# Kernel tuning notes

Hardware: AMD Instinct MI355X
Metric: run time of the kernel (lower is better)

Reference implementation:

```python
import jax, jax.numpy as jnp
import numpy as np
from itertools import product

DEG = 3
N_COMPLEX = 8

def monomial_powers(deg: int, n_complex: int = 8) -> np.ndarray:
    out = [a for a in product(range(deg + 1), repeat=n_complex) if sum(a) <= deg]
    return np.asarray(out, dtype=np.int32)

POWERS = monomial_powers(DEG, N_COMPLEX)  # (K, 8)
K = POWERS.shape[0]                       # 165 for deg=3
MAXP = int(POWERS.max())                  # 3


def z_monomials(q):
    """q (B,16) real -> z^alpha (B,K) complex, z_k = q[:,k] + i q[:,k+8]."""
    x, y = q[:, :N_COMPLEX], q[:, N_COMPLEX:]
    z = jax.lax.complex(x, y)  # (B, 8)
    # power ladders z^0..z^MAXP : (B, 8, MAXP+1)
    cur = jnp.ones_like(z)
    ladders = [cur]
    for _ in range(MAXP):
        cur = cur * z
        ladders.append(cur)
    lad = jnp.stack(ladders, axis=-1)  # (B, 8, MAXP+1)
    mon = jnp.ones((q.shape[0], K), dtype=z.dtype)
    for c in range(N_COMPLEX):  # fixed 8 iterations (structural)
        mon = mon * lad[:, c, POWERS[:, c]]  # gather (B, K)
    return mon


def setup_inputs() -> dict:
    key = jax.random.key(0)
    kq, = jax.random.split(key, 1)
    B = 262144
    q = jax.random.normal(kq, (B, 16), dtype=jnp.float32)
    L_re = jnp.eye(K, dtype=jnp.float32)
    L_im = jnp.zeros((K, K), dtype=jnp.float32)
    return {"q": q, "L_re": L_re, "L_im": L_im}


def reference(q, L_re, L_im):
    # Cholesky-like factor L: strict lower triangles + softplus-positive diagonal
    Lr = jnp.tril(L_re, -1)
    Li = jnp.tril(L_im, -1)
    diag = jax.nn.softplus(jnp.diagonal(L_re)) + 0.001
    L = jax.lax.complex(Lr, Li) + jnp.diag(jax.lax.complex(diag, jnp.zeros_like(diag)))
    H = L @ L.conj().T                      # (K, K) Hermitian PSD
    z_a = z_monomials(q)                    # (B, K) complex64
    Hs = z_a @ H.T                          # (B, K)
    quad = jnp.sum(Hs * jnp.conj(z_a), axis=-1).real  # (B,)
    return jnp.log(quad + 1e-12)
```

## Files before the change

kernel.cpp:

```cpp
#include <hip/hip_runtime.h>
#include <hip/hip_bf16.h>
#include <utility>

#define DEV static __device__ __forceinline__

typedef __attribute__((ext_vector_type(8))) short bf16x8;
typedef __attribute__((ext_vector_type(4))) float f32x4;

constexpr int KM   = 165;
constexpr int IT   = 11;
constexpr int ITP  = 12;
constexpr int KS   = 6;
constexpr int NB   = ITP * KS * 64;
constexpr int ROWS = 64;

struct Pw { unsigned char p[8]; };
struct PwTab { Pw a[KM]; };
constexpr PwTab gen_powers() {
  PwTab t{};
  int idx = 0;
  for (int a0 = 0; a0 <= 3; ++a0)
  for (int a1 = 0; a1 <= 3-a0; ++a1)
  for (int a2 = 0; a2 <= 3-a0-a1; ++a2)
  for (int a3 = 0; a3 <= 3-a0-a1-a2; ++a3)
  for (int a4 = 0; a4 <= 3-a0-a1-a2-a3; ++a4)
  for (int a5 = 0; a5 <= 3-a0-a1-a2-a3-a4; ++a5)
  for (int a6 = 0; a6 <= 3-a0-a1-a2-a3-a4-a5; ++a6)
  for (int a7 = 0; a7 <= 3-a0-a1-a2-a3-a4-a5-a6; ++a7) {
    t.a[idx].p[0] = (unsigned char)a0; t.a[idx].p[1] = (unsigned char)a1;
    t.a[idx].p[2] = (unsigned char)a2; t.a[idx].p[3] = (unsigned char)a3;
    t.a[idx].p[4] = (unsigned char)a4; t.a[idx].p[5] = (unsigned char)a5;
    t.a[idx].p[6] = (unsigned char)a6; t.a[idx].p[7] = (unsigned char)a7;
    ++idx;
  }
  return t;
}
constexpr PwTab PW = gen_powers();

DEV unsigned int f2bf(float f) {
  unsigned int u = __builtin_bit_cast(unsigned int, f);
  u += 0x7fffu + ((u >> 16) & 1u);
  return u >> 16;
}
DEV unsigned int pack2_bits(float lo, float hi) { return f2bf(lo) | (f2bf(hi) << 16); }
DEV unsigned int pack2(float lo, float hi) {
  unsigned int r;
  asm("v_cvt_pk_bf16_f32 %0, %1, %2" : "=v"(r) : "v"(lo), "v"(hi));
  return r;
}
DEV float softplusf(float x) { return (x > 20.f) ? x : log1pf(expf(x)); }

template<int JJ, int C>
DEV void mono_step(float& r, float& i,
                   const float (&lx)[8][3], const float (&ly)[8][3]) {
  constexpr int pc = PW.a[JJ].p[C];
  if constexpr (pc > 0) {
    const float ar = lx[C][pc-1], ai = ly[C][pc-1];
    const float tr = r*ar - i*ai;
    i = r*ai + i*ar;
    r = tr;
  }
}
template<int JJ>
DEV void mono_eval(float& mr, float& mi,
                   const float (&lx)[8][3], const float (&ly)[8][3]) {
  float r = 1.f, i = 0.f;
  mono_step<JJ,0>(r,i,lx,ly); mono_step<JJ,1>(r,i,lx,ly);
  mono_step<JJ,2>(r,i,lx,ly); mono_step<JJ,3>(r,i,lx,ly);
  mono_step<JJ,4>(r,i,lx,ly); mono_step<JJ,5>(r,i,lx,ly);
  mono_step<JJ,6>(r,i,lx,ly); mono_step<JJ,7>(r,i,lx,ly);
  mr = r; mi = i;
}
template<int JJ>
DEV void mono_eval_guard(float& r, float& i,
                         const float (&lx)[8][3], const float (&ly)[8][3]) {
  if constexpr (JJ < KM) mono_eval<JJ>(r, i, lx, ly);
  else { r = 0.f; i = 0.f; }
}

template<int T, int... Us>
DEV void gen8(std::integer_sequence<int, Us...>, float (&mr)[8], float (&mi)[8],
              const float (&lx)[8][3], const float (&ly)[8][3]) {
  (mono_eval_guard<8*T + Us>(mr[Us], mi[Us], lx, ly), ...);
}
template<int T>
DEV void gen_chunk(const float (&lx)[8][3], const float (&ly)[8][3],
                   unsigned int* Xf, unsigned int* Yf, int mf, int r15) {
  constexpr int ksv = T >> 2;
  constexpr int gv  = T & 3;
  float mr[8], mi[8];
  gen8<T>(std::make_integer_sequence<int, 8>{}, mr, mi, lx, ly);
  uint4 ux, uy;
  ux.x = pack2(mr[0], mr[1]); ux.y = pack2(mr[2], mr[3]);
  ux.z = pack2(mr[4], mr[5]); ux.w = pack2(mr[6], mr[7]);
  uy.x = pack2(mi[0], mi[1]); uy.y = pack2(mi[2], mi[3]);
  uy.z = pack2(mi[4], mi[5]); uy.w = pack2(mi[6], mi[7]);
  const unsigned int off = (unsigned int)((mf*6 + ksv)*256 + gv*64 + r15*4);
  *(uint4*)&Xf[off] = ux;
  *(uint4*)&Yf[off] = uy;
}
template<int W, int... Ts>
DEV void gen_seq(std::integer_sequence<int, Ts...>,
                 const float (&lx)[8][3], const float (&ly)[8][3],
                 unsigned int* Xf, unsigned int* Yf, int mf, int r15) {
  (gen_chunk<6*W + Ts>(lx, ly, Xf, Yf, mf, r15), ...);
}
template<int W>
DEV void gen_wave(const float (&lx)[8][3], const float (&ly)[8][3],
                  unsigned int* Xf, unsigned int* Yf, int mf, int r15) {
  gen_seq<W>(std::make_integer_sequence<int, 6>{}, lx, ly, Xf, Yf, mf, r15);
}

__global__ void __launch_bounds__(256) poskahler_prep(
    const float* __restrict__ Lre, const float* __restrict__ Lim,
    uint4* __restrict__ bp, uint4* __restrict__ bq) {
  const int tid = blockIdx.x * 256 + threadIdx.x;
  if (tid >= NB) return;
  const int lane = tid & 63;
  const int it = (tid >> 6) / KS;
  const int ks = (tid >> 6) % KS;
  const int j  = it * 16 + (lane & 15);
  const int ib = ks * 32 + ((lane >> 4) << 3);
  float pr[8], qr[8];
#pragma unroll
  for (int e = 0; e < 8; ++e) { pr[e] = 0.f; qr[e] = 0.f; }
  if (j < KM) {
#pragma unroll
    for (int e = 0; e < 8; ++e) {
      const int i = ib + e;
      if (i < KM) {
        if (i > j)      { pr[e] = Lre[i*KM + j]; qr[e] = -Lim[i*KM + j]; }
        else if (i == j){ pr[e] = softplusf(Lre[j*KM + j]) + 0.001f; }
      }
    }
  }
  uint4 up, uq;
  up.x = pack2_bits(pr[0], pr[1]); up.y = pack2_bits(pr[2], pr[3]);
  up.z = pack2_bits(pr[4], pr[5]); up.w = pack2_bits(pr[6], pr[7]);
  uq.x = pack2_bits(qr[0], qr[1]); uq.y = pack2_bits(qr[2], qr[3]);
  uq.z = pack2_bits(qr[4], qr[5]); uq.w = pack2_bits(qr[6], qr[7]);
  bp[tid] = up;
  bq[tid] = uq;
}

template<int KSv>
DEV void load_tiles(const uint4* __restrict__ bp, const uint4* __restrict__ bq,
                    int wv, int lane, uint4 (&tp)[3], uint4 (&tq)[3]) {
#pragma unroll
  for (int ii = 0; ii < 3; ++ii) {
    const int it = 4*ii + wv;
    if (it <= 2*KSv + 1 && it < IT) {
      const int fs = (it*KS + KSv)*64 + lane;
      tp[ii] = bp[fs];
      tq[ii] = bq[fs];
    }
  }
}

template<int KSv>
DEV void compute_ks(const unsigned int* Xf, const unsigned int* Yf,
                    int wv, int lane,
                    const uint4 (&tp)[3], const uint4 (&tq)[3],
                    float (&aRe)[3][4][4], float (&aIm)[3][4][4]) {
  bf16x8 xf[4], yf[4];
#pragma unroll
  for (int mf = 0; mf < 4; ++mf) {
    const unsigned int off = (unsigned int)((mf*6 + KSv)*256) + (unsigned int)lane*4;
    xf[mf] = __builtin_bit_cast(bf16x8, *(const uint4*)&Xf[off]);
    yf[mf] = __builtin_bit_cast(bf16x8, *(const uint4*)&Yf[off]);
  }
#pragma unroll
  for (int ii = 0; ii < 3; ++ii) {
    const int it = 4*ii + wv;
    if (it <= 2*KSv + 1 && it < IT) {
      const uint4 up = tp[ii];
      const uint4 uq = tq[ii];
      uint4 un;
      un.x = uq.x ^ 0x80008000u; un.y = uq.y ^ 0x80008000u;
      un.z = uq.z ^ 0x80008000u; un.w = uq.w ^ 0x80008000u;
      const bf16x8 vp = __builtin_bit_cast(bf16x8, up);
      const bf16x8 vq = __builtin_bit_cast(bf16x8, uq);
      const bf16x8 vn = __builtin_bit_cast(bf16x8, un);
#pragma unroll
      for (int mf = 0; mf < 4; ++mf) {
        f32x4 cre = { aRe[ii][mf][0], aRe[ii][mf][1], aRe[ii][mf][2], aRe[ii][mf][3] };
        f32x4 cim = { aIm[ii][mf][0], aIm[ii][mf][1], aIm[ii][mf][2], aIm[ii][mf][3] };
        cre = __builtin_amdgcn_mfma_f32_16x16x32_bf16(xf[mf], vp, cre, 0, 0, 0);
        cre = __builtin_amdgcn_mfma_f32_16x16x32_bf16(yf[mf], vq, cre, 0, 0, 0);
        cim = __builtin_amdgcn_mfma_f32_16x16x32_bf16(yf[mf], vp, cim, 0, 0, 0);
        cim = __builtin_amdgcn_mfma_f32_16x16x32_bf16(xf[mf], vn, cim, 0, 0, 0);
#pragma unroll
        for (int rr = 0; rr < 4; ++rr) { aRe[ii][mf][rr] = cre[rr]; aIm[ii][mf][rr] = cim[rr]; }
      }
    }
  }
}

__global__ void __launch_bounds__(256, 2) poskahler_main(
    const float* __restrict__ q,
    const uint4* __restrict__ bp, const uint4* __restrict__ bq,
    float* __restrict__ out) {
  __shared__ __align__(16) unsigned int Xf[6144];
  __shared__ __align__(16) unsigned int Yf[6144];
  __shared__ float qpart[4][ROWS];

  const int t     = threadIdx.x;
  const int lane  = t & 63;
  const int wv    = t >> 6;
  const int bbase = blockIdx.x * ROWS;
  const int mf_r  = lane >> 4;
  const int r15   = lane & 15;

  const float* qr = q + (size_t)(bbase + lane) * 16;
  const float4 q0 = ((const float4*)qr)[0];
  const float4 q1 = ((const float4*)qr)[1];
  const float4 q2 = ((const float4*)qr)[2];
  const float4 q3 = ((const float4*)qr)[3];

  uint4 tpA[3] = {}, tqA[3] = {}, tpB[3] = {}, tqB[3] = {};
  load_tiles<0>(bp, bq, wv, lane, tpA, tqA);
  load_tiles<1>(bp, bq, wv, lane, tpB, tqB);

  {
    const float xs[8] = {q0.x,q0.y,q0.z,q0.w,q1.x,q1.y,q1.z,q1.w};
    const float ys[8] = {q2.x,q2.y,q2.z,q2.w,q3.x,q3.y,q3.z,q3.w};
    float lx[8][3], ly[8][3];
#pragma unroll
    for (int c = 0; c < 8; ++c) {
      const float xr = xs[c], yi = ys[c];
      lx[c][0] = xr;             ly[c][0] = yi;
      lx[c][1] = xr*xr - yi*yi;  ly[c][1] = 2.f*xr*yi;
      lx[c][2] = lx[c][1]*xr - ly[c][1]*yi;
      ly[c][2] = lx[c][1]*yi + ly[c][1]*xr;
    }
    switch (wv) {
      case 0: gen_wave<0>(lx, ly, Xf, Yf, mf_r, r15); break;
      case 1: gen_wave<1>(lx, ly, Xf, Yf, mf_r, r15); break;
      case 2: gen_wave<2>(lx, ly, Xf, Yf, mf_r, r15); break;
      default: gen_wave<3>(lx, ly, Xf, Yf, mf_r, r15); break;
    }
  }
  __syncthreads();

  float aRe[3][4][4], aIm[3][4][4];
#pragma unroll
  for (int ii = 0; ii < 3; ++ii)
#pragma unroll
    for (int mf = 0; mf < 4; ++mf)
#pragma unroll
      for (int rr = 0; rr < 4; ++rr) { aRe[ii][mf][rr] = 0.f; aIm[ii][mf][rr] = 0.f; }

  compute_ks<0>(Xf, Yf, wv, lane, tpA, tqA, aRe, aIm);
  load_tiles<2>(bp, bq, wv, lane, tpA, tqA);
  compute_ks<1>(Xf, Yf, wv, lane, tpB, tqB, aRe, aIm);
  load_tiles<3>(bp, bq, wv, lane, tpB, tqB);
  compute_ks<2>(Xf, Yf, wv, lane, tpA, tqA, aRe, aIm);
  load_tiles<4>(bp, bq, wv, lane, tpA, tqA);
  compute_ks<3>(Xf, Yf, wv, lane, tpB, tqB, aRe, aIm);
  load_tiles<5>(bp, bq, wv, lane, tpB, tqB);
  compute_ks<4>(Xf, Yf, wv, lane, tpA, tqA, aRe, aIm);
  compute_ks<5>(Xf, Yf, wv, lane, tpB, tqB, aRe, aIm);

  float p[4][4];
#pragma unroll
  for (int mf = 0; mf < 4; ++mf)
#pragma unroll
    for (int rr = 0; rr < 4; ++rr) p[mf][rr] = 0.f;

#pragma unroll
  for (int ii = 0; ii < 3; ++ii)
#pragma unroll
    for (int mf = 0; mf < 4; ++mf)
#pragma unroll
      for (int rr = 0; rr < 4; ++rr)
        p[mf][rr] += aRe[ii][mf][rr]*aRe[ii][mf][rr] + aIm[ii][mf][rr]*aIm[ii][mf][rr];

#pragma unroll
  for (int mf = 0; mf < 4; ++mf)
#pragma unroll
    for (int rr = 0; rr < 4; ++rr) {
      float v = p[mf][rr];
      v += __shfl_xor(v, 1);
      v += __shfl_xor(v, 2);
      v += __shfl_xor(v, 4);
      v += __shfl_xor(v, 8);
      p[mf][rr] = v;
    }

  if (r15 == 0) {
    const int g = lane >> 4;
#pragma unroll
    for (int mf = 0; mf < 4; ++mf)
#pragma unroll
      for (int rr = 0; rr < 4; ++rr)
        qpart[wv][mf*16 + 4*g + rr] = p[mf][rr];
  }
  __syncthreads();
  if (t < ROWS) {
    const float quad = qpart[0][t] + qpart[1][t] + qpart[2][t] + qpart[3][t];
    out[bbase + t] = logf(quad + 1e-12f);
  }
}

extern "C" void kernel_launch(void* const* d_in, const int* in_sizes, int n_in,
                              void* d_out, int out_size, void* d_ws, size_t ws_size,
                              hipStream_t stream) {
  const float* q   = (const float*)d_in[0];
  const float* Lre = (const float*)d_in[1];
  const float* Lim = (const float*)d_in[2];
  float* out = (float*)d_out;
  uint4* bp = (uint4*)d_ws;
  uint4* bq = bp + NB;
  const int B = in_sizes[0] / 16;
  poskahler_prep<<<(NB + 255)/256, 256, 0, stream>>>(Lre, Lim, bp, bq);
  poskahler_main<<<B / ROWS, 256, 0, stream>>>(q, bp, bq, out);
}
```

Baseline: 52.20 us.

## Rebalance triangular tile work per wave and stream tiles to cut registers

Swaps the interleaved per-wave assignment of 11 column tiles over 6 k-steps for a compile-time work queue per wave. Each wave now processes its tiles one at a time, with a single set of accumulators that is reduced into the quadratic sum and cleared at each tile boundary. Tile loads are double-buffered two steps ahead, and launch bounds rise to 3 blocks per SM. The aim is to balance MFMA work across waves and cut accumulator register pressure for higher occupancy. In exchange, X/Y fragments are reloaded from LDS on every tile step instead of once per k-step.

Result: slower. 60.01 us (+14.9%).

```diff
diff --git a/kernel.cpp b/kernel.cpp
--- a/kernel.cpp
+++ b/kernel.cpp
@@ -143,60 +143,82 @@
   bq[tid] = uq;
 }
 
-template<int KSv>
-DEV void load_tiles(const uint4* __restrict__ bp, const uint4* __restrict__ bq,
-                    int wv, int lane, uint4 (&tp)[3], uint4 (&tq)[3]) {
-#pragma unroll
-  for (int ii = 0; ii < 3; ++ii) {
-    const int it = 4*ii + wv;
-    if (it <= 2*KSv + 1 && it < IT) {
-      const int fs = (it*KS + KSv)*64 + lane;
-      tp[ii] = bp[fs];
-      tq[ii] = bq[fs];
-    }
-  }
-}
-
-template<int KSv>
-DEV void compute_ks(const unsigned int* Xf, const unsigned int* Yf,
-                    int wv, int lane,
-                    const uint4 (&tp)[3], const uint4 (&tq)[3],
-                    float (&aRe)[3][4][4], float (&aIm)[3][4][4]) {
-  bf16x8 xf[4], yf[4];
+struct WQ { int n; signed char it[11]; signed char ks[11]; };
+constexpr WQ WQP[4] = {
+  {11, {0,0,0,0,0,0, 7,7,7, 8,8},    {0,1,2,3,4,5, 3,4,5, 4,5}},
+  {11, {1,1,1,1,1,1, 6,6,6, 9,9},    {0,1,2,3,4,5, 3,4,5, 4,5}},
+  {10, {2,2,2,2,2, 4,4,4,4, 10,-1},  {1,2,3,4,5, 2,3,4,5, 5,-1}},
+  {9,  {3,3,3,3,3, 5,5,5,5,-1,-1},   {1,2,3,4,5, 2,3,4,5,-1,-1}},
+};
+
+template<int W>
+DEV void preload(const uint4* __restrict__ bp, const uint4* __restrict__ bq,
+                 int lane, uint4 (&tP)[2], uint4 (&tQ)[2]) {
+  constexpr int f0 = (WQP[W].it[0]*KS + WQP[W].ks[0]) * 64;
+  constexpr int f1 = (WQP[W].it[1]*KS + WQP[W].ks[1]) * 64;
+  tP[0] = bp[f0 + lane]; tQ[0] = bq[f0 + lane];
+  tP[1] = bp[f1 + lane]; tQ[1] = bq[f1 + lane];
+}
+
+template<int W, int I>
+DEV void tile_step(const unsigned int* Xf, const unsigned int* Yf,
+                   const uint4* __restrict__ bp, const uint4* __restrict__ bq,
+                   int lane, uint4 (&tP)[2], uint4 (&tQ)[2],
+                   f32x4 (&aRe)[4], f32x4 (&aIm)[4], float (&p)[4][4]) {
+  constexpr int ks = WQP[W].ks[I];
+  const uint4 up = tP[I & 1];
+  const uint4 uq = tQ[I & 1];
+  if constexpr (I + 2 < WQP[W].n) {
+    constexpr int fs0 = (WQP[W].it[I+2]*KS + WQP[W].ks[I+2]) * 64;
+    tP[I & 1] = bp[fs0 + lane];
+    tQ[I & 1] = bq[fs0 + lane];
+  }
+  uint4 un;
+  un.x = uq.x ^ 0x80008000u; un.y = uq.y ^ 0x80008000u;
+  un.z = uq.z ^ 0x80008000u; un.w = uq.w ^ 0x80008000u;
+  const bf16x8 vp = __builtin_bit_cast(bf16x8, up);
+  const bf16x8 vq = __builtin_bit_cast(bf16x8, uq);
+  const bf16x8 vn = __builtin_bit_cast(bf16x8, un);
 #pragma unroll
   for (int mf = 0; mf < 4; ++mf) {
-    const unsigned int off = (unsigned int)((mf*6 + KSv)*256) + (unsigned int)lane*4;
-    xf[mf] = __builtin_bit_cast(bf16x8, *(const uint4*)&Xf[off]);
-    yf[mf] = __builtin_bit_cast(bf16x8, *(const uint4*)&Yf[off]);
-  }
-#pragma unroll
-  for (int ii = 0; ii < 3; ++ii) {
-    const int it = 4*ii + wv;
-    if (it <= 2*KSv + 1 && it < IT) {
-      const uint4 up = tp[ii];
-      const uint4 uq = tq[ii];
-      uint4 un;
-      un.x = uq.x ^ 0x80008000u; un.y = uq.y ^ 0x80008000u;
-      un.z = uq.z ^ 0x80008000u; un.w = uq.w ^ 0x80008000u;
-      const bf16x8 vp = __builtin_bit_cast(bf16x8, up);
-      const bf16x8 vq = __builtin_bit_cast(bf16x8, uq);
-      const bf16x8 vn = __builtin_bit_cast(bf16x8, un);
-#pragma unroll
-      for (int mf = 0; mf < 4; ++mf) {
-        f32x4 cre = { aRe[ii][mf][0], aRe[ii][mf][1], aRe[ii][mf][2], aRe[ii][mf][3] };
-        f32x4 cim = { aIm[ii][mf][0], aIm[ii][mf][1], aIm[ii][mf][2], aIm[ii][mf][3] };
-        cre = __builtin_amdgcn_mfma_f32_16x16x32_bf16(xf[mf], vp, cre, 0, 0, 0);
-        cre = __builtin_amdgcn_mfma_f32_16x16x32_bf16(yf[mf], vq, cre, 0, 0, 0);
-        cim = __builtin_amdgcn_mfma_f32_16x16x32_bf16(yf[mf], vp, cim, 0, 0, 0);
-        cim = __builtin_amdgcn_mfma_f32_16x16x32_bf16(xf[mf], vn, cim, 0, 0, 0);
-#pragma unroll
-        for (int rr = 0; rr < 4; ++rr) { aRe[ii][mf][rr] = cre[rr]; aIm[ii][mf][rr] = cim[rr]; }
-      }
-    }
-  }
-}
-
-__global__ void __launch_bounds__(256, 2) poskahler_main(
+    const unsigned int off = (unsigned int)((mf*6 + ks)*256) + (unsigned int)lane*4;
+    const bf16x8 xf = __builtin_bit_cast(bf16x8, *(const uint4*)&Xf[off]);
+    const bf16x8 yf = __builtin_bit_cast(bf16x8, *(const uint4*)&Yf[off]);
+    aRe[mf] = __builtin_amdgcn_mfma_f32_16x16x32_bf16(xf, vp, aRe[mf], 0, 0, 0);
+    aRe[mf] = __builtin_amdgcn_mfma_f32_16x16x32_bf16(yf, vq, aRe[mf], 0, 0, 0);
+    aIm[mf] = __builtin_amdgcn_mfma_f32_16x16x32_bf16(yf, vp, aIm[mf], 0, 0, 0);
+    aIm[mf] = __builtin_amdgcn_mfma_f32_16x16x32_bf16(xf, vn, aIm[mf], 0, 0, 0);
+  }
+  if constexpr (I + 1 == WQP[W].n || WQP[W].it[I+1] != WQP[W].it[I]) {
+#pragma unroll
+    for (int mf = 0; mf < 4; ++mf) {
+#pragma unroll
+      for (int rr = 0; rr < 4; ++rr)
+        p[mf][rr] += aRe[mf][rr]*aRe[mf][rr] + aIm[mf][rr]*aIm[mf][rr];
+      aRe[mf] = (f32x4){0.f,0.f,0.f,0.f};
+      aIm[mf] = (f32x4){0.f,0.f,0.f,0.f};
+    }
+  }
+}
+
+template<int W, int... Is>
+DEV void run_tiles(std::integer_sequence<int, Is...>,
+                   const unsigned int* Xf, const unsigned int* Yf,
+                   const uint4* __restrict__ bp, const uint4* __restrict__ bq,
+                   int lane, uint4 (&tP)[2], uint4 (&tQ)[2],
+                   f32x4 (&aRe)[4], f32x4 (&aIm)[4], float (&p)[4][4]) {
+  (tile_step<W, Is>(Xf, Yf, bp, bq, lane, tP, tQ, aRe, aIm, p), ...);
+}
+template<int W>
+DEV void run_wave(const unsigned int* Xf, const unsigned int* Yf,
+                  const uint4* __restrict__ bp, const uint4* __restrict__ bq,
+                  int lane, uint4 (&tP)[2], uint4 (&tQ)[2],
+                  f32x4 (&aRe)[4], f32x4 (&aIm)[4], float (&p)[4][4]) {
+  run_tiles<W>(std::make_integer_sequence<int, WQP[W].n>{},
+               Xf, Yf, bp, bq, lane, tP, tQ, aRe, aIm, p);
+}
+
+__global__ void __launch_bounds__(256, 3) poskahler_main(
     const float* __restrict__ q,
     const uint4* __restrict__ bp, const uint4* __restrict__ bq,
     float* __restrict__ out) {
@@ -217,9 +239,13 @@
   const float4 q2 = ((const float4*)qr)[2];
   const float4 q3 = ((const float4*)qr)[3];
 
-  uint4 tpA[3] = {}, tqA[3] = {}, tpB[3] = {}, tqB[3] = {};
-  load_tiles<0>(bp, bq, wv, lane, tpA, tqA);
-  load_tiles<1>(bp, bq, wv, lane, tpB, tqB);
+  uint4 tP[2], tQ[2];
+  switch (wv) {
+    case 0: preload<0>(bp, bq, lane, tP, tQ); break;
+    case 1: preload<1>(bp, bq, lane, tP, tQ); break;
+    case 2: preload<2>(bp, bq, lane, tP, tQ); break;
+    default: preload<3>(bp, bq, lane, tP, tQ); break;
+  }
 
   {
     const float xs[8] = {q0.x,q0.y,q0.z,q0.w,q1.x,q1.y,q1.z,q1.w};
@@ -242,38 +268,24 @@
   }
   __syncthreads();
 
-  float aRe[3][4][4], aIm[3][4][4];
-#pragma unroll
-  for (int ii = 0; ii < 3; ++ii)
-#pragma unroll
-    for (int mf = 0; mf < 4; ++mf)
-#pragma unroll
-      for (int rr = 0; rr < 4; ++rr) { aRe[ii][mf][rr] = 0.f; aIm[ii][mf][rr] = 0.f; }
-
-  compute_ks<0>(Xf, Yf, wv, lane, tpA, tqA, aRe, aIm);
-  load_tiles<2>(bp, bq, wv, lane, tpA, tqA);
-  compute_ks<1>(Xf, Yf, wv, lane, tpB, tqB, aRe, aIm);
-  load_tiles<3>(bp, bq, wv, lane, tpB, tqB);
-  compute_ks<2>(Xf, Yf, wv, lane, tpA, tqA, aRe, aIm);
-  load_tiles<4>(bp, bq, wv, lane, tpA, tqA);
-  compute_ks<3>(Xf, Yf, wv, lane, tpB, tqB, aRe, aIm);
-  load_tiles<5>(bp, bq, wv, lane, tpB, tqB);
-  compute_ks<4>(Xf, Yf, wv, lane, tpA, tqA, aRe, aIm);
-  compute_ks<5>(Xf, Yf, wv, lane, tpB, tqB, aRe, aIm);
-
+  f32x4 aRe[4], aIm[4];
+#pragma unroll
+  for (int mf = 0; mf < 4; ++mf) {
+    aRe[mf] = (f32x4){0.f,0.f,0.f,0.f};
+    aIm[mf] = (f32x4){0.f,0.f,0.f,0.f};
+  }
   float p[4][4];
 #pragma unroll
   for (int mf = 0; mf < 4; ++mf)
 #pragma unroll
     for (int rr = 0; rr < 4; ++rr) p[mf][rr] = 0.f;
 
-#pragma unroll
-  for (int ii = 0; ii < 3; ++ii)
-#pragma unroll
-    for (int mf = 0; mf < 4; ++mf)
-#pragma unroll
-      for (int rr = 0; rr < 4; ++rr)
-        p[mf][rr] += aRe[ii][mf][rr]*aRe[ii][mf][rr] + aIm[ii][mf][rr]*aIm[ii][mf][rr];
+  switch (wv) {
+    case 0: run_wave<0>(Xf, Yf, bp, bq, lane, tP, tQ, aRe, aIm, p); break;
+    case 1: run_wave<1>(Xf, Yf, bp, bq, lane, tP, tQ, aRe, aIm, p); break;
+    case 2: run_wave<2>(Xf, Yf, bp, bq, lane, tP, tQ, aRe, aIm, p); break;
+    default: run_wave<3>(Xf, Yf, bp, bq, lane, tP, tQ, aRe, aIm, p); break;
+  }
 
 #pragma unroll
   for (int mf = 0; mf < 4; ++mf)
```
